# Kernel optimization log

Measured on AMD Instinct MI355X. Metric: run time of the kernel, lower is better.

## Reference

```python
import jax, jax.numpy as jnp
import numpy as np

B, H, T = 32, 48, 24
S, A, R, F, L = 256, 64, 8, 1024, 2
EPS = 1e-5


def setup_inputs() -> dict:
    key = jax.random.key(0)
    ks = jax.random.split(key, 12)
    def w(k, shape):
        fan_in = shape[-1]
        return jax.random.normal(k, shape, jnp.float32) / jnp.sqrt(jnp.float32(fan_in))
    return {
        'history_s': jax.random.normal(ks[0], (B, H, S), jnp.float32),
        'history_a': jax.random.normal(ks[1], (B, H, A), jnp.float32),
        'present_s': jax.random.normal(ks[2], (B, S), jnp.float32),
        'future_s': jax.random.normal(ks[3], (B, T, S), jnp.float32),
        'future_a': jax.random.normal(ks[4], (B, T, A), jnp.float32),
        'W_state': w(ks[5], (F, S)), 'b_state': jnp.zeros((F,), jnp.float32),
        'g_sn': jnp.ones((F,), jnp.float32), 'b_sn': jnp.zeros((F,), jnp.float32),
        'W_action': w(ks[6], (F, A)), 'b_action': jnp.zeros((F,), jnp.float32),
        'g_an': jnp.ones((F,), jnp.float32), 'b_an': jnp.zeros((F,), jnp.float32),
        'gru_Wi': w(ks[7], (L, 3 * F, F)), 'gru_Wh': w(ks[8], (L, 3 * F, F)),
        'gru_bi': jnp.zeros((L, 3 * F), jnp.float32), 'gru_bh': jnp.zeros((L, 3 * F), jnp.float32),
        'W_reward': w(ks[9], (R, F)), 'b_reward': jnp.zeros((R,), jnp.float32),
        'W_sout': w(ks[10], (S, F)), 'b_sout': jnp.zeros((S,), jnp.float32),
    }


def _ln(x, g, b):
    m = jnp.mean(x, axis=-1, keepdims=True)
    v = jnp.mean(jnp.square(x - m), axis=-1, keepdims=True)
    return (x - m) / jnp.sqrt(v + EPS) * g + b


def _gelu(x):
    return jax.nn.gelu(x, approximate=False)  # torch F.gelu default = exact erf


def _gru_step(Wi, Wh, bi, bh, hs, x):
    # hs: [L,B,F] hidden per layer; x: [B,F]. PyTorch GRU cell semantics.
    new_hs = []
    inp = x
    for l in range(Wi.shape[0]):
        gi = inp @ Wi[l].T + bi[l]      # [B,3F]
        gh = hs[l] @ Wh[l].T + bh[l]    # [B,3F]
        ir, iz, inn = jnp.split(gi, 3, axis=-1)
        hr, hz, hn = jnp.split(gh, 3, axis=-1)
        r = jax.nn.sigmoid(ir + hr)
        z = jax.nn.sigmoid(iz + hz)
        n = jnp.tanh(inn + r * hn)
        h_new = (1.0 - z) * n + z * hs[l]
        new_hs.append(h_new)
        inp = h_new  # dropout between layers is identity (drop_rate=0)
    return jnp.stack(new_hs), inp


def reference(history_s, history_a, present_s, future_s, future_a,
              W_state, b_state, g_sn, b_sn, W_action, b_action, g_an, b_an,
              gru_Wi, gru_Wh, gru_bi, gru_bh, W_reward, b_reward, W_sout, b_sout):
    # Original forward() reruns the GRU from scratch over a growing window each
    # future step; since h0=0 this is mathematically identical to carrying the
    # hidden state incrementally (module's own _forward variant), which we do.
    Bv = history_s.shape[0]
    Fv = W_state.shape[0]
    Lv = gru_Wi.shape[0]

    hs = _ln(history_s @ W_state.T + b_state, g_sn, b_sn)   # [B,H,F]
    ha = _ln(history_a @ W_action.T + b_action, g_an, b_an)  # [B,H,F]
    ps = _ln(present_s @ W_state.T + b_state, g_sn, b_sn)    # [B,F]
    fa = _ln(future_a @ W_action.T + b_action, g_an, b_an)   # [B,T,F]

    hist_sa = hs + ha  # [B,H,F]

    def head(y):
        r = jnp.tanh(y @ W_reward.T + b_reward)
        s = y @ W_sout.T + b_sout  # state_activation is identity
        return r, s

    # step 0: full window = history + (present + future_a[0])
    seq0 = _gelu(jnp.concatenate([hist_sa, (ps + fa[:, 0])[:, None, :]], axis=1))
    h0 = jnp.zeros((Lv, Bv, Fv), seq0.dtype)

    def scan_seq(h, x):
        h, y = _gru_step(gru_Wi, gru_Wh, gru_bi, gru_bh, h, x)
        return h, y

    hT, ys = jax.lax.scan(scan_seq, h0, jnp.swapaxes(seq0, 0, 1))  # ys: [H+1,B,F]
    r0, s0 = head(ys[-1])
    pres = _ln(s0 @ W_state.T + b_state, g_sn, b_sn)

    def scan_fut(carry, fa_t):
        h, p = carry
        x = _gelu(p + fa_t)  # [B,F]
        h, y = _gru_step(gru_Wi, gru_Wh, gru_bi, gru_bh, h, x)
        r, s = head(y)
        p_new = _ln(s @ W_state.T + b_state, g_sn, b_sn)
        return (h, p_new), (r, s)

    _, (rs, ss) = jax.lax.scan(scan_fut, (hT, pres), jnp.swapaxes(fa[:, 1:], 0, 1))
    future_r = jnp.concatenate([r0[:, None], jnp.swapaxes(rs, 0, 1)], axis=1)  # [B,T,R]
    future_s_out = jnp.concatenate([s0[:, None], jnp.swapaxes(ss, 0, 1)], axis=1)  # [B,T,S]
    return future_r, future_s_out
```

## Files before the change

### kernel.cpp

```cpp
#include <hip/hip_runtime.h>
#include <cmath>

constexpr int kB = 32, kH = 48, kT = 24, kS = 256, kA = 64, kR = 8, kF = 1024;
constexpr int kSEQ = kH + 1;
constexpr float kEPS = 1e-5f;

constexpr int G  = 128;
constexpr int BT = 512;

constexpr int GRPS = 8;
constexpr int GMEM = 16;

typedef __attribute__((ext_vector_type(8))) short short8;
typedef __attribute__((ext_vector_type(4))) float f32x4;

union U4S8 { uint4 u; short8 s; };

__device__ __forceinline__ unsigned bfbits(float x) {
  unsigned u = __float_as_uint(x);
  return (u + 0x7fffu + ((u >> 16) & 1u)) >> 16;
}
__device__ __forceinline__ float bf_lo(unsigned u) { return __uint_as_float(u << 16); }
__device__ __forceinline__ float bf_hi(unsigned u) { return __uint_as_float(u & 0xffff0000u); }
__device__ __forceinline__ float bf2f(unsigned short h) {
  return __uint_as_float(((unsigned)h) << 16);
}
__device__ __forceinline__ float gelu_f(float x) {
  return 0.5f * x * (1.0f + erff(x * 0.7071067811865476f));
}
__device__ __forceinline__ float sigmoid_f(float x) {
  return 1.0f / (1.0f + expf(-x));
}

__device__ __forceinline__ void coh_st(unsigned* p, unsigned v) {
  __hip_atomic_store(p, v, __ATOMIC_RELAXED, __HIP_MEMORY_SCOPE_AGENT);
}

__device__ __forceinline__ unsigned poll_ld(const unsigned* p) {
  unsigned v;
  asm volatile("global_load_dword %0, %1, off sc0 sc1\n\t"
               "s_waitcnt vmcnt(0)"
               : "=v"(v) : "v"(p) : "memory");
  return v;
}

__device__ __forceinline__ void sync_grid(unsigned* bar, int grp, int& t) {
  __syncthreads();
  if (threadIdx.x == 0) {
    const unsigned tt = (unsigned)t;
    unsigned* garr = bar + grp * 32;
    unsigned* root = bar + GRPS * 32;
    unsigned* grel = bar + (GRPS + 1) * 32 + grp * 32;
    const unsigned old = __hip_atomic_fetch_add(
        garr, 1u, __ATOMIC_RELAXED, __HIP_MEMORY_SCOPE_AGENT);
    if (old == (unsigned)GMEM * tt - 1u) {
      const unsigned rold = __hip_atomic_fetch_add(
          root, 1u, __ATOMIC_RELAXED, __HIP_MEMORY_SCOPE_AGENT);
      if (rold != (unsigned)GRPS * tt - 1u) {
        while (poll_ld(root) < (unsigned)GRPS * tt) { }
      }
      __hip_atomic_fetch_add(grel, 1u, __ATOMIC_RELAXED,
                             __HIP_MEMORY_SCOPE_AGENT);
    } else {
      while (poll_ld(grel) < tt) { }
    }
  }
  __syncthreads();
  t++;
}

__device__ __forceinline__ void layer_stage(
    const unsigned short* __restrict__ xsrc,
    const unsigned short* __restrict__ hsrc,
    unsigned short* __restrict__ hdst,
    const short8 (&Bf)[2][3][4],
    float bR, float bZ, float bIN, float bHN,
    float& h_old, float* part, int fb)
{
  const int tid = threadIdx.x;
  const int wv = tid >> 6, l = tid & 63, q = l >> 4, c = l & 15;

  short8 Afr[2][2][4];
  #pragma unroll
  for (int mt = 0; mt < 2; mt++)
    #pragma unroll
    for (int j = 0; j < 4; j++) {
      const int off = (mt*16 + c)*1024 + wv*128 + j*32 + q*8;
      Afr[0][mt][j] = *(const short8*)(xsrc + off);
      Afr[1][mt][j] = *(const short8*)(hsrc + off);
    }

  f32x4 C[4][2];
  #pragma unroll
  for (int s = 0; s < 4; s++)
    #pragma unroll
    for (int mt = 0; mt < 2; mt++)
      C[s][mt] = (f32x4){0.f, 0.f, 0.f, 0.f};

  #pragma unroll
  for (int mt = 0; mt < 2; mt++)
    #pragma unroll
    for (int j = 0; j < 4; j++) {
      C[0][mt] = __builtin_amdgcn_mfma_f32_16x16x32_bf16(Afr[0][mt][j], Bf[0][0][j], C[0][mt], 0, 0, 0);
      C[0][mt] = __builtin_amdgcn_mfma_f32_16x16x32_bf16(Afr[1][mt][j], Bf[1][0][j], C[0][mt], 0, 0, 0);
      C[1][mt] = __builtin_amdgcn_mfma_f32_16x16x32_bf16(Afr[0][mt][j], Bf[0][1][j], C[1][mt], 0, 0, 0);
      C[1][mt] = __builtin_amdgcn_mfma_f32_16x16x32_bf16(Afr[1][mt][j], Bf[1][1][j], C[1][mt], 0, 0, 0);
      C[2][mt] = __builtin_amdgcn_mfma_f32_16x16x32_bf16(Afr[0][mt][j], Bf[0][2][j], C[2][mt], 0, 0, 0);
      C[3][mt] = __builtin_amdgcn_mfma_f32_16x16x32_bf16(Afr[1][mt][j], Bf[1][2][j], C[3][mt], 0, 0, 0);
    }

  const int perm = (wv + l + (l >> 3)) & 7;
  #pragma unroll
  for (int s = 0; s < 4; s++)
    #pragma unroll
    for (int mt = 0; mt < 2; mt++)
      #pragma unroll
      for (int r = 0; r < 4; r++)
        part[((s*2 + mt)*4 + r)*512 + l*8 + perm] = C[s][mt][r];
  __syncthreads();

  const int mt_c = wv & 1, rg = wv >> 1;
  const int b_own = mt_c*16 + q*4 + rg;
  float S[4];
  #pragma unroll
  for (int s = 0; s < 4; s++) {
    const float* pp = part + ((s*2 + mt_c)*4 + rg)*512 + l*8;
    f32x4 a = *(const f32x4*)pp;
    f32x4 b = *(const f32x4*)(pp + 4);
    S[s] = ((a[0]+a[1]) + (a[2]+a[3])) + ((b[0]+b[1]) + (b[2]+b[3]));
  }
  float rr = sigmoid_f(S[0] + bR);
  float zz = sigmoid_f(S[1] + bZ);
  float nn = tanhf(S[2] + bIN + rr * (S[3] + bHN));
  float hn = (1.f - zz)*nn + zz*h_old;
  h_old = hn;
  float nb = __shfl_xor(hn, 1);
  if (!(c & 1)) {
    unsigned pk = bfbits(hn) | (bfbits(nb) << 16);
    coh_st((unsigned*)(hdst + b_own*1024 + fb*16 + c), pk);
  }
  __syncthreads();
}

__device__ __forceinline__ void f3_stage(
    const unsigned short* __restrict__ y_bf, int t,
    const unsigned short* __restrict__ WsT2_bf, const float* __restrict__ b_sout,
    const unsigned short* __restrict__ Wr_bf, const float* __restrict__ b_reward,
    const unsigned short* __restrict__ WstT_bf, const float* __restrict__ b_state,
    const float* __restrict__ g_sn, const float* __restrict__ b_sn,
    const unsigned short* __restrict__ fa_bf,
    float* __restrict__ out_r, float* __restrict__ out_s,
    unsigned short* __restrict__ xbuf_bf, float* part, int b)
{
  const int tid = threadIdx.x;
  float* yb    = part;
  float* spart = part + 1024;
  float* s_sh  = part + 1536;
  float* rpart = part + 1792;
  float* red1  = part + 2048;
  float* red2  = part + 2560;

  {
    unsigned uu = *((const unsigned*)y_bf + b*512 + tid);
    yb[tid*2]     = bf_lo(uu);
    yb[tid*2 + 1] = bf_hi(uu);
  }
  __syncthreads();
  {
    const int j = tid & 255, ksh = tid >> 8;
    const unsigned* wp = (const unsigned*)WsT2_bf + (size_t)ksh*256*256 + j;
    const float* yp = yb + ksh*512;
    float acc = 0.f;
    #pragma unroll 8
    for (int kp = 0; kp < 256; kp++) {
      unsigned w = wp[kp*256];
      acc += bf_lo(w)*yp[2*kp] + bf_hi(w)*yp[2*kp + 1];
    }
    spart[tid] = acc;
  }
  __syncthreads();
  if (tid < 256) {
    float s = spart[tid] + spart[tid + 256] + b_sout[tid];
    out_s[((size_t)b*kT + t)*kS + tid] = s;
    s_sh[tid] = s;
  } else if (tid < 320) {
    const int idx = tid - 256, j = idx >> 3, ks = idx & 7;
    const unsigned short* wr = Wr_bf + j*1024 + ks*128;
    const float* yp = yb + ks*128;
    float acc = 0.f;
    #pragma unroll 4
    for (int k = 0; k < 128; k += 2) {
      unsigned w = *(const unsigned*)(wr + k);
      acc += bf_lo(w)*yp[k] + bf_hi(w)*yp[k+1];
    }
    rpart[idx] = acc;
  }
  __syncthreads();
  if (tid < 8) {
    float a = b_reward[tid];
    #pragma unroll
    for (int ks = 0; ks < 8; ks++) a += rpart[tid*8 + ks];
    out_r[((size_t)b*kT + t)*kR + tid] = tanhf(a);
  }
  if (t == kT - 1) return;
  __syncthreads();
  const int f0 = tid*2;
  float a0 = b_state[f0], a1 = b_state[f0 + 1];
  {
    const unsigned* wp = (const unsigned*)WstT_bf + (f0 >> 1);
    #pragma unroll 8
    for (int k = 0; k < 256; k++) {
      unsigned w = wp[k*512];
      a0 += bf_lo(w)*s_sh[k];
      a1 += bf_hi(w)*s_sh[k];
    }
  }
  float s1 = a0 + a1, s2 = a0*a0 + a1*a1;
  red1[tid] = s1; red2[tid] = s2;
  __syncthreads();
  for (int off = 256; off > 0; off >>= 1) {
    if (tid < off) { red1[tid] += red1[tid + off]; red2[tid] += red2[tid + off]; }
    __syncthreads();
  }
  const float mean = red1[0] * (1.0f/kF);
  const float var  = red2[0] * (1.0f/kF) - mean*mean;
  const float inv  = rsqrtf(var + kEPS);
  unsigned fu = *((const unsigned*)(fa_bf + ((size_t)(t+1)*kB + b)*kF) + tid);
  float x0 = (a0 - mean)*inv*g_sn[f0]   + b_sn[f0]   + bf_lo(fu);
  float x1 = (a1 - mean)*inv*g_sn[f0+1] + b_sn[f0+1] + bf_hi(fu);
  unsigned pk = bfbits(gelu_f(x0)) | (bfbits(gelu_f(x1)) << 16);
  coh_st((unsigned*)xbuf_bf + b*512 + tid, pk);
}

__device__ __forceinline__ void load_bfrags(
    const float* __restrict__ gru_Wi, const float* __restrict__ gru_Wh,
    int lay, int fb, int wv, int q, int c, short8 (&Bf)[2][3][4])
{
  const size_t WLL = (size_t)3 * kF * kF;
  const float* Wm[2] = { gru_Wi + lay*WLL, gru_Wh + lay*WLL };
  #pragma unroll
  for (int m = 0; m < 2; m++)
    #pragma unroll
    for (int g = 0; g < 3; g++)
      #pragma unroll
      for (int j = 0; j < 4; j++) {
        const float* p = Wm[m] + ((size_t)(g*kF + fb*16 + c))*kF + wv*128 + j*32 + q*8;
        float4 a = *(const float4*)p;
        float4 b = *(const float4*)(p + 4);
        U4S8 u;
        u.u.x = bfbits(a.x) | (bfbits(a.y) << 16);
        u.u.y = bfbits(a.z) | (bfbits(a.w) << 16);
        u.u.z = bfbits(b.x) | (bfbits(b.y) << 16);
        u.u.w = bfbits(b.z) | (bfbits(b.w) << 16);
        Bf[m][g][j] = u.s;
      }
}

__global__ __launch_bounds__(BT, 2) void gru_hist(
    const float* __restrict__ gru_Wi, const float* __restrict__ gru_Wh,
    const float* __restrict__ gru_bi, const float* __restrict__ gru_bh,
    const unsigned short* __restrict__ seq0_bf,
    unsigned short* h0pool, unsigned short* h1pool,
    unsigned* cnt)
{
  __shared__ float part[32 * 512];
  const int tid = threadIdx.x;
  const int blk = blockIdx.x;
  const int wv = tid >> 6, l = tid & 63, q = l >> 4, c = l & 15;
  const bool isL1 = (blk >= 64);
  const int fb = blk & 63;
  const int grp = blk >> 4;
  const int lay = isL1 ? 1 : 0;
  const size_t BF = (size_t)kB * kF;

  short8 Bf[2][3][4];
  load_bfrags(gru_Wi, gru_Wh, lay, fb, wv, q, c, Bf);
  const int f = fb*16 + c;
  const float* bi = gru_bi + lay*3*kF;
  const float* bh = gru_bh + lay*3*kF;
  const float bR  = bi[f] + bh[f];
  const float bZ  = bi[kF + f] + bh[kF + f];
  const float bIN = bi[2*kF + f];
  const float bHN = bh[2*kF + f];

  float h_old = 0.f;
  int tg = 1;

  #define H0P(i) (h0pool + (size_t)(i)*BF)
  #define H1P(i) (h1pool + (size_t)(i)*BF)
  for (int s = 0; s < 50; s++) {
    if (!isL1) {
      if (s < 49)
        layer_stage(seq0_bf + (size_t)s*BF, H0P(s), H0P(s+1),
                    Bf, bR, bZ, bIN, bHN, h_old, part, fb);
    } else {
      if (s >= 1)
        layer_stage(H0P(s), H1P(s-1), H1P(s),
                    Bf, bR, bZ, bIN, bHN, h_old, part, fb);
    }
    if (s < 49) sync_grid(cnt, grp, tg);
  }
  #undef H0P
  #undef H1P
}

__global__ __launch_bounds__(BT, 2) void gru_fut(
    const float* __restrict__ gru_Wi, const float* __restrict__ gru_Wh,
    const float* __restrict__ gru_bi, const float* __restrict__ gru_bh,
    const unsigned short* __restrict__ WsT2_bf, const float* __restrict__ b_sout,
    const unsigned short* __restrict__ Wr_bf, const float* __restrict__ b_reward,
    const unsigned short* __restrict__ WstT_bf, const float* __restrict__ b_state,
    const float* __restrict__ g_sn, const float* __restrict__ b_sn,
    const unsigned short* __restrict__ fa_bf,
    unsigned short* h0pool, unsigned short* h1pool, unsigned short* xbpool,
    unsigned* cnt,
    float* __restrict__ out_r, float* __restrict__ out_s)
{
  __shared__ float part[32 * 512];
  const int tid = threadIdx.x;
  const int blk = blockIdx.x;
  const int wv = tid >> 6, l = tid & 63, q = l >> 4, c = l & 15;
  const bool isL1 = (blk >= 64);
  const int fb = blk & 63;
  const int grp = blk >> 4;
  const int lay = isL1 ? 1 : 0;
  const size_t BF = (size_t)kB * kF;

  short8 Bf[2][3][4];
  load_bfrags(gru_Wi, gru_Wh, lay, fb, wv, q, c, Bf);
  const int f = fb*16 + c;
  const float* bi = gru_bi + lay*3*kF;
  const float* bh = gru_bh + lay*3*kF;
  const float bR  = bi[f] + bh[f];
  const float bZ  = bi[kF + f] + bh[kF + f];
  const float bIN = bi[2*kF + f];
  const float bHN = bh[2*kF + f];

  #define H0P(i) (h0pool + (size_t)(i)*BF)
  #define H1P(i) (h1pool + (size_t)(i)*BF)
  #define XBP(i) (xbpool + (size_t)(i)*BF)

  const int b_own = (wv & 1)*16 + q*4 + (wv >> 1);
  float h_old;
  {
    const unsigned short* hs = isL1 ? H1P(49) : H0P(49);
    h_old = bf2f(hs[b_own*1024 + f]);
  }
  int tg = 1;

  for (int t = 0; t < kT; t++) {
    if (blk < kB)
      f3_stage(H1P(49+t), t, WsT2_bf, b_sout, Wr_bf, b_reward,
               WstT_bf, b_state, g_sn, b_sn, fa_bf,
               out_r, out_s, XBP(t), part, blk);
    if (t == kT - 1) break;
    sync_grid(cnt, grp, tg);
    if (!isL1)
      layer_stage(XBP(t), H0P(49+t), H0P(50+t),
                  Bf, bR, bZ, bIN, bHN, h_old, part, fb);
    sync_grid(cnt, grp, tg);
    if (isL1)
      layer_stage(H0P(50+t), H1P(49+t), H1P(50+t),
                  Bf, bR, bZ, bIN, bHN, h_old, part, fb);
    sync_grid(cnt, grp, tg);
  }
  #undef H0P
  #undef H1P
  #undef XBP
}

__global__ __launch_bounds__(512) void convert_weights(
    const float* __restrict__ ws,  unsigned short* __restrict__ wsT2,
    const float* __restrict__ wst, unsigned short* __restrict__ wstT,
    const float* __restrict__ wr,  unsigned short* __restrict__ o3)
{
  const int stride = gridDim.x * blockDim.x;
  const int i0 = blockIdx.x * blockDim.x + threadIdx.x;
  for (int i = i0; i < kS*kF; i += stride) {
    const int j = i >> 10, k = i & 1023;
    wsT2[(k >> 1)*512 + j*2 + (k & 1)] = (unsigned short)bfbits(ws[i]);
  }
  for (int i = i0; i < kF*kS; i += stride) {
    const int ff = i >> 8, k = i & 255;
    wstT[k*1024 + ff] = (unsigned short)bfbits(wst[i]);
  }
  for (int i = i0; i < kR*kF; i += stride) o3[i] = (unsigned short)bfbits(wr[i]);
}

__global__ __launch_bounds__(256) void encode_fa_kernel(
    const float* __restrict__ future_a,
    const float* __restrict__ W_action, const float* __restrict__ b_action,
    const float* __restrict__ g_an, const float* __restrict__ b_an,
    unsigned short* __restrict__ fa_bf)
{
  __shared__ __align__(16) float arow[kA];
  __shared__ float red1[256], red2[256];
  const int bid = blockIdx.x;
  const int b = bid & (kB - 1);
  const int t = bid >> 5;
  const int tid = threadIdx.x;
  if (tid < kA) arow[tid] = future_a[((size_t)b*kT + t)*kA + tid];
  __syncthreads();
  float v[4]; float s1 = 0.f, s2 = 0.f;
  #pragma unroll
  for (int j = 0; j < 4; j++) {
    const int ff = tid + j*256;
    const float* wr = W_action + (size_t)ff*kA;
    float acc = b_action[ff];
    for (int k = 0; k < kA; k += 4) {
      float4 w  = *(const float4*)(wr + k);
      float4 xv = *(const float4*)(arow + k);
      acc += xv.x*w.x + xv.y*w.y + xv.z*w.z + xv.w*w.w;
    }
    v[j] = acc; s1 += acc; s2 += acc*acc;
  }
  red1[tid] = s1; red2[tid] = s2;
  __syncthreads();
  for (int off = 128; off > 0; off >>= 1) {
    if (tid < off) { red1[tid] += red1[tid+off]; red2[tid] += red2[tid+off]; }
    __syncthreads();
  }
  const float m = red1[0] * (1.0f/kF);
  const float va = red2[0] * (1.0f/kF) - m*m;
  const float inv = rsqrtf(va + kEPS);
  #pragma unroll
  for (int j = 0; j < 4; j++) {
    const int ff = tid + j*256;
    fa_bf[((size_t)t*kB + b)*kF + ff] =
        (unsigned short)bfbits((v[j] - m)*inv*g_an[ff] + b_an[ff]);
  }
}

__global__ __launch_bounds__(256) void encode_seq0_kernel(
    const float* __restrict__ history_s, const float* __restrict__ history_a,
    const float* __restrict__ present_s,
    const float* __restrict__ W_state, const float* __restrict__ b_state,
    const float* __restrict__ g_sn, const float* __restrict__ b_sn,
    const float* __restrict__ W_action, const float* __restrict__ b_action,
    const float* __restrict__ g_an, const float* __restrict__ b_an,
    const unsigned short* __restrict__ fa_bf, unsigned short* __restrict__ seq0_bf)
{
  __shared__ __align__(16) float srow[kS];
  __shared__ __align__(16) float arow[kA];
  __shared__ float red1[256], red2[256];
  const int bid = blockIdx.x;
  const int b = bid & (kB - 1);
  const int t = bid >> 5;
  const int tid = threadIdx.x;
  const bool hist = (t < kH);
  const float* sp = hist ? (history_s + ((size_t)b*kH + t)*kS)
                         : (present_s + (size_t)b*kS);
  srow[tid] = sp[tid];
  if (hist && tid < kA) arow[tid] = history_a[((size_t)b*kH + t)*kA + tid];
  __syncthreads();

  float u[4]; float s1 = 0.f, s2 = 0.f;
  #pragma unroll
  for (int j = 0; j < 4; j++) {
    const int ff = tid + j*256;
    const float* wr = W_state + (size_t)ff*kS;
    float acc = b_state[ff];
    for (int k = 0; k < kS; k += 4) {
      float4 w  = *(const float4*)(wr + k);
      float4 xv = *(const float4*)(srow + k);
      acc += xv.x*w.x + xv.y*w.y + xv.z*w.z + xv.w*w.w;
    }
    u[j] = acc; s1 += acc; s2 += acc*acc;
  }
  red1[tid] = s1; red2[tid] = s2;
  __syncthreads();
  for (int off = 128; off > 0; off >>= 1) {
    if (tid < off) { red1[tid] += red1[tid+off]; red2[tid] += red2[tid+off]; }
    __syncthreads();
  }
  const float mu = red1[0] * (1.0f/kF);
  const float vu = red2[0] * (1.0f/kF) - mu*mu;
  const float iu = rsqrtf(vu + kEPS);
  __syncthreads();

  if (hist) {
    float v[4]; s1 = 0.f; s2 = 0.f;
    #pragma unroll
    for (int j = 0; j < 4; j++) {
      const int ff = tid + j*256;
      const float* wr = W_action + (size_t)ff*kA;
      float acc = b_action[ff];
      for (int k = 0; k < kA; k += 4) {
        float4 w  = *(const float4*)(wr + k);
        float4 xv = *(const float4*)(arow + k);
        acc += xv.x*w.x + xv.y*w.y + xv.z*w.z + xv.w*w.w;
      }
      v[j] = acc; s1 += acc; s2 += acc*acc;
    }
    red1[tid] = s1; red2[tid] = s2;
    __syncthreads();
    for (int off = 128; off > 0; off >>= 1) {
      if (tid < off) { red1[tid] += red1[tid+off]; red2[tid] += red2[tid+off]; }
      __syncthreads();
    }
    const float mv = red1[0] * (1.0f/kF);
    const float vv = red2[0] * (1.0f/kF) - mv*mv;
    const float iv = rsqrtf(vv + kEPS);
    #pragma unroll
    for (int j = 0; j < 4; j++) {
      const int ff = tid + j*256;
      const float un = (u[j] - mu)*iu*g_sn[ff] + b_sn[ff];
      const float vn = (v[j] - mv)*iv*g_an[ff] + b_an[ff];
      seq0_bf[((size_t)t*kB + b)*kF + ff] = (unsigned short)bfbits(gelu_f(un + vn));
    }
  } else {
    #pragma unroll
    for (int j = 0; j < 4; j++) {
      const int ff = tid + j*256;
      const float un = (u[j] - mu)*iu*g_sn[ff] + b_sn[ff];
      seq0_bf[((size_t)t*kB + b)*kF + ff] =
          (unsigned short)bfbits(gelu_f(un + bf2f(fa_bf[(size_t)b*kF + ff])));
    }
  }
}

extern "C" void kernel_launch(void* const* d_in, const int* in_sizes, int n_in,
                              void* d_out, int out_size, void* d_ws, size_t ws_size,
                              hipStream_t stream) {
  (void)in_sizes; (void)n_in; (void)out_size;
  const float* history_s = (const float*)d_in[0];
  const float* history_a = (const float*)d_in[1];
  const float* present_s = (const float*)d_in[2];
  const float* future_a  = (const float*)d_in[4];
  const float* W_state   = (const float*)d_in[5];
  const float* b_state   = (const float*)d_in[6];
  const float* g_sn      = (const float*)d_in[7];
  const float* b_sn      = (const float*)d_in[8];
  const float* W_action  = (const float*)d_in[9];
  const float* b_action  = (const float*)d_in[10];
  const float* g_an      = (const float*)d_in[11];
  const float* b_an      = (const float*)d_in[12];
  const float* gru_Wi    = (const float*)d_in[13];
  const float* gru_Wh    = (const float*)d_in[14];
  const float* gru_bi    = (const float*)d_in[15];
  const float* gru_bh    = (const float*)d_in[16];
  const float* W_reward  = (const float*)d_in[17];
  const float* b_reward  = (const float*)d_in[18];
  const float* W_sout    = (const float*)d_in[19];
  const float* b_sout    = (const float*)d_in[20];

  char* ws = (char*)d_ws;
  unsigned short* seq0_bf = (unsigned short*)(ws + 0);
  unsigned short* fa_bf   = (unsigned short*)(ws + 3211264);
  unsigned short* WsT2_bf = (unsigned short*)(ws + 4784128);
  unsigned short* WstT_bf = (unsigned short*)(ws + 5308416);
  unsigned short* Wr_bf   = (unsigned short*)(ws + 5832704);
  unsigned short* h0pool  = (unsigned short*)(ws + 5849088);
  unsigned short* h1pool  = (unsigned short*)(ws + 10633216);
  unsigned short* xbpool  = (unsigned short*)(ws + 15417344);
  unsigned*       cnt     = (unsigned*)(ws + 16924672);
  const size_t need = 16929280;
  if (ws_size < need) return;

  hipMemsetAsync((void*)h0pool, 0, 65536, stream);
  hipMemsetAsync((void*)h1pool, 0, 65536, stream);
  hipMemsetAsync((void*)cnt, 0, 4608, stream);

  float* out_r = (float*)d_out;
  float* out_s = out_r + (size_t)kB*kT*kR;

  hipLaunchKernelGGL(convert_weights, dim3(256), dim3(512), 0, stream,
                     W_sout, WsT2_bf, W_state, WstT_bf, W_reward, Wr_bf);
  hipLaunchKernelGGL(encode_fa_kernel, dim3(kT*kB), dim3(256), 0, stream,
                     future_a, W_action, b_action, g_an, b_an, fa_bf);
  hipLaunchKernelGGL(encode_seq0_kernel, dim3(kSEQ*kB), dim3(256), 0, stream,
                     history_s, history_a, present_s,
                     W_state, b_state, g_sn, b_sn,
                     W_action, b_action, g_an, b_an, fa_bf, seq0_bf);
  hipLaunchKernelGGL(gru_hist, dim3(G), dim3(BT), 0, stream,
                     gru_Wi, gru_Wh, gru_bi, gru_bh,
                     seq0_bf, h0pool, h1pool, cnt);
  hipLaunchKernelGGL(gru_fut, dim3(G), dim3(BT), 0, stream,
                     gru_Wi, gru_Wh, gru_bi, gru_bh,
                     WsT2_bf, b_sout, Wr_bf, b_reward, WstT_bf, b_state,
                     g_sn, b_sn, fa_bf,
                     h0pool, h1pool, xbpool, cnt + 576,
                     out_r, out_s);
}
```

Measured before the change: 1.556 ms.

## Replace grid-wide barriers with per-step dataflow flags between GRU layers

Replaces the hierarchical grid barrier after every step with per-timestep counters. Each block group signals completion of its layer slice and consumers wait only on the flags they depend on, polling four group counters at once. Layer 0 and layer 1 blocks can now run skewed in the pipeline without all 128 blocks meeting at every step, which is meant to cut barrier latency and idle time. Memory ordering relies on relaxed atomics after __syncthreads plus coherent loads, which risks visibility races.

```diff
diff --git a/kernel.cpp b/kernel.cpp
--- a/kernel.cpp
+++ b/kernel.cpp
@@ -7,9 +7,6 @@
 
 constexpr int G  = 128;
 constexpr int BT = 512;
-
-constexpr int GRPS = 8;
-constexpr int GMEM = 16;
 
 typedef __attribute__((ext_vector_type(8))) short short8;
 typedef __attribute__((ext_vector_type(4))) float f32x4;
@@ -36,37 +33,30 @@
   __hip_atomic_store(p, v, __ATOMIC_RELAXED, __HIP_MEMORY_SCOPE_AGENT);
 }
 
-__device__ __forceinline__ unsigned poll_ld(const unsigned* p) {
-  unsigned v;
-  asm volatile("global_load_dword %0, %1, off sc0 sc1\n\t"
-               "s_waitcnt vmcnt(0)"
-               : "=v"(v) : "v"(p) : "memory");
-  return v;
-}
-
-__device__ __forceinline__ void sync_grid(unsigned* bar, int grp, int& t) {
-  __syncthreads();
+__device__ __forceinline__ void sig(unsigned* fl, int grp) {
+  if (threadIdx.x == 0)
+    __hip_atomic_fetch_add(fl + (grp & 3) * 32, 1u,
+                           __ATOMIC_RELAXED, __HIP_MEMORY_SCOPE_AGENT);
+}
+__device__ __forceinline__ void wait4(const unsigned* fl,
+                                      unsigned t0, unsigned t1,
+                                      unsigned t2, unsigned t3) {
   if (threadIdx.x == 0) {
-    const unsigned tt = (unsigned)t;
-    unsigned* garr = bar + grp * 32;
-    unsigned* root = bar + GRPS * 32;
-    unsigned* grel = bar + (GRPS + 1) * 32 + grp * 32;
-    const unsigned old = __hip_atomic_fetch_add(
-        garr, 1u, __ATOMIC_RELAXED, __HIP_MEMORY_SCOPE_AGENT);
-    if (old == (unsigned)GMEM * tt - 1u) {
-      const unsigned rold = __hip_atomic_fetch_add(
-          root, 1u, __ATOMIC_RELAXED, __HIP_MEMORY_SCOPE_AGENT);
-      if (rold != (unsigned)GRPS * tt - 1u) {
-        while (poll_ld(root) < (unsigned)GRPS * tt) { }
-      }
-      __hip_atomic_fetch_add(grel, 1u, __ATOMIC_RELAXED,
-                             __HIP_MEMORY_SCOPE_AGENT);
-    } else {
-      while (poll_ld(grel) < tt) { }
-    }
-  }
-  __syncthreads();
-  t++;
+    for (;;) {
+      unsigned a, b, c, d;
+      asm volatile(
+        "global_load_dword %0, %4, off sc0 sc1\n\t"
+        "global_load_dword %1, %5, off sc0 sc1\n\t"
+        "global_load_dword %2, %6, off sc0 sc1\n\t"
+        "global_load_dword %3, %7, off sc0 sc1\n\t"
+        "s_waitcnt vmcnt(0)"
+        : "=&v"(a), "=&v"(b), "=&v"(c), "=&v"(d)
+        : "v"(fl), "v"(fl + 32), "v"(fl + 64), "v"(fl + 96)
+        : "memory");
+      if (a >= t0 && b >= t1 && c >= t2 && d >= t3) break;
+    }
+  }
+  __syncthreads();
 }
 
 __device__ __forceinline__ void layer_stage(
@@ -261,7 +251,7 @@
     const float* __restrict__ gru_bi, const float* __restrict__ gru_bh,
     const unsigned short* __restrict__ seq0_bf,
     unsigned short* h0pool, unsigned short* h1pool,
-    unsigned* cnt)
+    unsigned* hflags)
 {
   __shared__ float part[32 * 512];
   const int tid = threadIdx.x;
@@ -284,24 +274,34 @@
   const float bHN = bh[2*kF + f];
 
   float h_old = 0.f;
-  int tg = 1;
 
   #define H0P(i) (h0pool + (size_t)(i)*BF)
   #define H1P(i) (h1pool + (size_t)(i)*BF)
+  #define FH0(s) (hflags + (size_t)((s) - 1) * 128)
+  #define FH1(s) (hflags + (size_t)(49 + (s) - 1) * 128)
+
   for (int s = 0; s < 50; s++) {
     if (!isL1) {
-      if (s < 49)
+      if (s < 49) {
+        if (s >= 1) wait4(FH0(s), 16, 16, 16, 16);
         layer_stage(seq0_bf + (size_t)s*BF, H0P(s), H0P(s+1),
                     Bf, bR, bZ, bIN, bHN, h_old, part, fb);
+        sig(FH0(s+1), grp);
+      }
     } else {
-      if (s >= 1)
+      if (s >= 1) {
+        wait4(FH0(s), 16, 16, 16, 16);
+        if (s >= 2) wait4(FH1(s-1), 16, 16, 16, 16);
         layer_stage(H0P(s), H1P(s-1), H1P(s),
                     Bf, bR, bZ, bIN, bHN, h_old, part, fb);
-    }
-    if (s < 49) sync_grid(cnt, grp, tg);
+        sig(FH1(s), grp);
+      }
+    }
   }
   #undef H0P
   #undef H1P
+  #undef FH0
+  #undef FH1
 }
 
 __global__ __launch_bounds__(BT, 2) void gru_fut(
@@ -313,7 +313,7 @@
     const float* __restrict__ g_sn, const float* __restrict__ b_sn,
     const unsigned short* __restrict__ fa_bf,
     unsigned short* h0pool, unsigned short* h1pool, unsigned short* xbpool,
-    unsigned* cnt,
+    unsigned* fflags,
     float* __restrict__ out_r, float* __restrict__ out_s)
 {
   __shared__ float part[32 * 512];
@@ -339,6 +339,9 @@
   #define H0P(i) (h0pool + (size_t)(i)*BF)
   #define H1P(i) (h1pool + (size_t)(i)*BF)
   #define XBP(i) (xbpool + (size_t)(i)*BF)
+  #define FXF(t)  (fflags + (size_t)(t) * 128)
+  #define FH0F(t) (fflags + (size_t)(23 + (t)) * 128)
+  #define FH1F(t) (fflags + (size_t)(46 + (t)) * 128)
 
   const int b_own = (wv & 1)*16 + q*4 + (wv >> 1);
   float h_old;
@@ -346,27 +349,36 @@
     const unsigned short* hs = isL1 ? H1P(49) : H0P(49);
     h_old = bf2f(hs[b_own*1024 + f]);
   }
-  int tg = 1;
 
   for (int t = 0; t < kT; t++) {
-    if (blk < kB)
+    if (blk < kB) {
+      if (t >= 1) wait4(FH1F(t-1), 16, 16, 16, 16);
       f3_stage(H1P(49+t), t, WsT2_bf, b_sout, Wr_bf, b_reward,
                WstT_bf, b_state, g_sn, b_sn, fa_bf,
                out_r, out_s, XBP(t), part, blk);
+      if (t < kT - 1) { __syncthreads(); sig(FXF(t), grp); }
+    }
     if (t == kT - 1) break;
-    sync_grid(cnt, grp, tg);
-    if (!isL1)
+    if (!isL1) {
+      wait4(FXF(t), 16, 16, 0, 0);
+      if (t >= 1) wait4(FH0F(t-1), 16, 16, 16, 16);
       layer_stage(XBP(t), H0P(49+t), H0P(50+t),
                   Bf, bR, bZ, bIN, bHN, h_old, part, fb);
-    sync_grid(cnt, grp, tg);
-    if (isL1)
+      sig(FH0F(t), grp);
+    } else {
+      wait4(FH0F(t), 16, 16, 16, 16);
+      if (t >= 1) wait4(FH1F(t-1), 16, 16, 16, 16);
       layer_stage(H0P(50+t), H1P(49+t), H1P(50+t),
                   Bf, bR, bZ, bIN, bHN, h_old, part, fb);
-    sync_grid(cnt, grp, tg);
+      sig(FH1F(t), grp);
+    }
   }
   #undef H0P
   #undef H1P
   #undef XBP
+  #undef FXF
+  #undef FH0F
+  #undef FH1F
 }
 
 __global__ __launch_bounds__(512) void convert_weights(
@@ -553,13 +565,14 @@
   unsigned short* h0pool  = (unsigned short*)(ws + 5849088);
   unsigned short* h1pool  = (unsigned short*)(ws + 10633216);
   unsigned short* xbpool  = (unsigned short*)(ws + 15417344);
-  unsigned*       cnt     = (unsigned*)(ws + 16924672);
-  const size_t need = 16929280;
+  unsigned*       hflags  = (unsigned*)(ws + 16924672);
+  unsigned*       fflags  = (unsigned*)(ws + 16974848);
+  const size_t need = 17010176;
   if (ws_size < need) return;
 
   hipMemsetAsync((void*)h0pool, 0, 65536, stream);
   hipMemsetAsync((void*)h1pool, 0, 65536, stream);
-  hipMemsetAsync((void*)cnt, 0, 4608, stream);
+  hipMemsetAsync((void*)hflags, 0, 50176 + 35328, stream);
 
   float* out_r = (float*)d_out;
   float* out_s = out_r + (size_t)kB*kT*kR;
@@ -574,11 +587,11 @@
                      W_action, b_action, g_an, b_an, fa_bf, seq0_bf);
   hipLaunchKernelGGL(gru_hist, dim3(G), dim3(BT), 0, stream,
                      gru_Wi, gru_Wh, gru_bi, gru_bh,
-                     seq0_bf, h0pool, h1pool, cnt);
+                     seq0_bf, h0pool, h1pool, hflags);
   hipLaunchKernelGGL(gru_fut, dim3(G), dim3(BT), 0, stream,
                      gru_Wi, gru_Wh, gru_bi, gru_bh,
                      WsT2_bf, b_sout, Wr_bf, b_reward, WstT_bf, b_state,
                      g_sn, b_sn, fa_bf,
-                     h0pool, h1pool, xbpool, cnt + 576,
+                     h0pool, h1pool, xbpool, fflags,
                      out_r, out_s);
 }
```

Result: no change. 1.582 ms (+1.7%).
